# Kernel tuning notes

Hardware: AMD Instinct MI355X
Metric: run time of the kernel (lower is better)

## Reference

```python
import jax, jax.numpy as jnp
import numpy as np

NUM_HEADS = 16
HEAD_DIM = 64  # hidden_size 1024 / 16 heads


def setup_inputs() -> dict:
    key = jax.random.key(0)
    ks = jax.random.split(key, 4)
    B, S, H = 2, 2048, 1024
    scale = 0.02
    return {
        "hidden_states": jax.random.normal(ks[0], (B, S, H), jnp.float32),
        "attention_mask": jnp.zeros((B, 1, 1, S), jnp.float32),  # additive mask
        "Wq": jax.random.normal(ks[1], (H, H), jnp.float32) * scale,
        "bq": jnp.zeros((H,), jnp.float32),
        "Wk": jax.random.normal(ks[2], (H, H), jnp.float32) * scale,
        "bk": jnp.zeros((H,), jnp.float32),
        "Wv": jax.random.normal(ks[3], (H, H), jnp.float32) * scale,
        "bv": jnp.zeros((H,), jnp.float32),
    }


def _split_heads(x):
    B, S, H = x.shape
    return x.reshape(B, S, NUM_HEADS, HEAD_DIM).transpose(0, 2, 1, 3)  # [B,h,S,dh]


def reference(hidden_states, attention_mask, Wq, bq, Wk, bk, Wv, bv):
    q = _split_heads(hidden_states @ Wq + bq)
    k = _split_heads(hidden_states @ Wk + bk)
    v = _split_heads(hidden_states @ Wv + bv)
    # scaled dot-product scores [B,h,S,S]
    scores = jnp.einsum("bhqd,bhkd->bhqk", q, k) / np.sqrt(HEAD_DIM).astype(np.float32)
    scores = scores + attention_mask  # additive mask, broadcast [B,1,1,S]
    probs = jax.nn.softmax(scores, axis=-1)  # dropout prob = 0.0
    ctx = jnp.einsum("bhqk,bhkd->bhqd", probs, v)
    B, h, S, dh = ctx.shape
    return ctx.transpose(0, 2, 1, 3).reshape(B, S, h * dh)  # [B,S,hidden]
```

## Files before the change

### kernel.cpp

```cpp
#include <hip/hip_runtime.h>
#include <hip/hip_bf16.h>


typedef __bf16 bf16x8 __attribute__((ext_vector_type(8)));
typedef __bf16 bf16x4 __attribute__((ext_vector_type(4)));
typedef float f32x4 __attribute__((ext_vector_type(4)));

static constexpr int H = 1024;
static constexpr int S = 2048;
static constexpr int NH = 16;
static constexpr int DH = 64;
static constexpr float L2E = 1.4426950408889634f;

#if __has_builtin(__builtin_amdgcn_exp2f)
#define EXP2F(x) __builtin_amdgcn_exp2f(x)
#else
#define EXP2F(x) __builtin_exp2f(x)
#endif

__device__ inline void gll16(const void* g, void* l) {
  __builtin_amdgcn_global_load_lds(
      (const __attribute__((address_space(1))) void*)g,
      (__attribute__((address_space(3))) void*)l, 16, 0, 0);
}

__global__ __launch_bounds__(256) void convert_kernel(
    const float* __restrict__ X, const float* __restrict__ W0,
    const float* __restrict__ W1, const float* __restrict__ W2,
    __bf16* __restrict__ Xb, __bf16* __restrict__ Wt) {
  __shared__ float T[64][65];
  const int bid = blockIdx.x, tid = threadIdx.x;
  if (bid < 2048) {
    size_t i = ((size_t)bid * 256 + tid) * 8;
    float4 f0 = *(const float4*)(X + i);
    float4 f1 = *(const float4*)(X + i + 4);
    bf16x8 o;
    o[0] = (__bf16)f0.x; o[1] = (__bf16)f0.y; o[2] = (__bf16)f0.z; o[3] = (__bf16)f0.w;
    o[4] = (__bf16)f1.x; o[5] = (__bf16)f1.y; o[6] = (__bf16)f1.z; o[7] = (__bf16)f1.w;
    *(bf16x8*)(Xb + i) = o;
    return;
  }
  const int wid = bid - 2048;
  const int z = wid >> 8, t = wid & 255;
  const int k0 = (t >> 4) * 64, n0 = (t & 15) * 64;
  const float* W = z == 0 ? W0 : (z == 1 ? W1 : W2);
  __bf16* Wo = Wt + (size_t)z * H * H;
#pragma unroll
  for (int it = 0; it < 4; ++it) {
    int r = it * 16 + (tid >> 4), c = (tid & 15) * 4;
    *(float4*)&T[r][c] = *(const float4*)&W[(size_t)(k0 + r) * H + n0 + c];
  }
  __syncthreads();
#pragma unroll
  for (int it = 0; it < 4; ++it) {
    int n = it * 16 + (tid >> 4), c0 = (tid & 15) * 4;
    bf16x4 o;
#pragma unroll
    for (int j = 0; j < 4; ++j) o[j] = (__bf16)T[c0 + j][n];
    *(bf16x4*)&Wo[(size_t)(n0 + n) * H + k0 + c0] = o;
  }
}

__global__ __launch_bounds__(256, 3) void qkv_gemm_kernel(
    const __bf16* __restrict__ Xb, const __bf16* __restrict__ Wt,
    const float* __restrict__ bq, const float* __restrict__ bk,
    const float* __restrict__ bv,
    __bf16* __restrict__ Q, __bf16* __restrict__ K, __bf16* __restrict__ Vt)
{
  __shared__ __bf16 smem[2 * 128 * 64];
  __bf16* As = smem;
  __bf16* Bs = smem + 128 * 64;

  const int tid = threadIdx.x, lane = tid & 63, w = tid >> 6;
  const int quad = lane >> 4, l16 = lane & 15;
  const int wsel = blockIdx.x >> 3;
  const int n0 = (blockIdx.x & 7) * 128;
  const int m0 = blockIdx.y * 128;
  const int wr = w & 1, wc = w >> 1;

  const __bf16* Wsel = Wt + (size_t)wsel * H * H;
  const float* bias = wsel == 0 ? bq : (wsel == 1 ? bk : bv);

  const __bf16* aptr[4];
  const __bf16* bptr[4];
#pragma unroll
  for (int i = 0; i < 4; ++i) {
    int s = w * 256 + i * 64 + lane;
    int row = s >> 3, col = s & 7, sc = col ^ (row & 7);
    aptr[i] = Xb + (size_t)(m0 + row) * H + sc * 8;
    bptr[i] = Wsel + (size_t)(n0 + row) * H + sc * 8;
  }

  f32x4 acc[4][4];
#pragma unroll
  for (int u = 0; u < 4; ++u) {
    float bv_ = bias[n0 + wc * 64 + u * 16 + l16];
#pragma unroll
    for (int t = 0; t < 4; ++t) acc[t][u] = {bv_, bv_, bv_, bv_};
  }

  for (int k0 = 0; k0 < H; k0 += 64) {
    __syncthreads();
#pragma unroll
    for (int i = 0; i < 4; ++i) {
      gll16(aptr[i] + k0, &As[(w * 256 + i * 64) * 8]);
      gll16(bptr[i] + k0, &Bs[(w * 256 + i * 64) * 8]);
    }
    __syncthreads();
#pragma unroll
    for (int kc = 0; kc < 2; ++kc) {
      bf16x8 af[4], bfr[4];
#pragma unroll
      for (int t = 0; t < 4; ++t) {
        int ra = wr * 64 + t * 16 + l16;
        af[t] = *(const bf16x8*)&As[ra * 64 + (((kc * 4 + quad) ^ (ra & 7)) * 8)];
        int rb = wc * 64 + t * 16 + l16;
        bfr[t] = *(const bf16x8*)&Bs[rb * 64 + (((kc * 4 + quad) ^ (rb & 7)) * 8)];
      }
#pragma unroll
      for (int t = 0; t < 4; ++t)
#pragma unroll
        for (int u = 0; u < 4; ++u)
          acc[t][u] = __builtin_amdgcn_mfma_f32_16x16x32_bf16(af[t], bfr[u], acc[t][u], 0, 0, 0);
    }
  }

  const int b = m0 >> 11;
  if (wsel <= 1) {
    __syncthreads();
    __bf16* Tr = smem + w * (64 * 64);
    const float scl = wsel == 0 ? 0.125f * L2E : 1.0f;
#pragma unroll
    for (int t = 0; t < 4; ++t)
#pragma unroll
      for (int u = 0; u < 4; ++u)
#pragma unroll
        for (int r = 0; r < 4; ++r) {
          int row = t * 16 + quad * 4 + r;
          int col = u * 16 + l16;
          Tr[row * 64 + (((col >> 3) ^ (row & 7)) * 8 + (col & 7))] =
              (__bf16)(acc[t][u][r] * scl);
        }
    const int head = (n0 + wc * 64) >> 6;
    const int bh = b * NH + head;
    const int si = (m0 & (S - 1)) + wr * 64 + lane;
    __bf16* dst = (wsel == 0 ? Q : K) + ((size_t)bh * S + si) * DH;
#pragma unroll
    for (int c = 0; c < 8; ++c)
      *(bf16x8*)&dst[c * 8] =
          *(const bf16x8*)&Tr[lane * 64 + ((c ^ (lane & 7)) * 8)];
  } else {
#pragma unroll
    for (int u = 0; u < 4; ++u) {
      int n = n0 + wc * 64 + u * 16 + l16;
      int head = n >> 6, d = n & 63;
#pragma unroll
      for (int t = 0; t < 4; ++t) {
        int srow = m0 + wr * 64 + t * 16 + quad * 4;
        int si = srow & (S - 1);
        int bh = b * NH + head;
        bf16x4 o;
#pragma unroll
        for (int r = 0; r < 4; ++r) o[r] = (__bf16)acc[t][u][r];
        *(bf16x4*)&Vt[((size_t)bh * DH + d) * S + si] = o;
      }
    }
  }
}

__global__ __launch_bounds__(512, 4) void attn_kernel(
    const __bf16* __restrict__ Q, const __bf16* __restrict__ K,
    const __bf16* __restrict__ Vt, const float* __restrict__ mask,
    float* __restrict__ out)
{
  __shared__ __bf16 Ks[128 * 64];
  __shared__ __bf16 Vs[64 * 128];
  __shared__ float  Ms[S];
  __shared__ __bf16 Pb[8][16][128];

  const int tid = threadIdx.x, lane = tid & 63, w = tid >> 6;
  const int quad = lane >> 4, l16 = lane & 15;
  const int bh = blockIdx.y, b = bh >> 4, h = bh & 15;
  const int q0 = blockIdx.x * 128;

  const __bf16* Qb = Q + (size_t)bh * S * DH;
  const __bf16* Kb = K + (size_t)bh * S * DH;
  const __bf16* Vb = Vt + (size_t)bh * DH * S;
  const float* mb = mask + (size_t)b * S;

  {
    int idx = tid * 4;
    float4 mv = *(const float4*)&mb[idx];
    float4 sv = {mv.x * L2E, mv.y * L2E, mv.z * L2E, mv.w * L2E};
    *(float4*)&Ms[idx] = sv;
  }

  const int q = q0 + w * 16 + l16;
  bf16x8 qf[2];
#pragma unroll
  for (int kc = 0; kc < 2; ++kc)
    qf[kc] = *(const bf16x8*)&Qb[(size_t)q * DH + kc * 32 + quad * 8];

  bf16x8 ones_frag;
#pragma unroll
  for (int j = 0; j < 8; ++j) ones_frag[j] = (l16 == 0) ? (__bf16)1.0f : (__bf16)0.0f;

  const __bf16* kptr[2];
  const __bf16* vptr[2];
#pragma unroll
  for (int i = 0; i < 2; ++i) {
    int s = i * 512 + tid;
    {
      int row = s >> 3, col = s & 7, sc = col ^ (row & 7);
      kptr[i] = Kb + (size_t)row * DH + sc * 8;
    }
    {
      int row = s >> 4, col = s & 15, sc = col ^ (row & 15);
      vptr[i] = Vb + (size_t)row * S + sc * 8;
    }
  }

  f32x4 o[4] = {};
  f32x4 o4 = {};

  for (int kv0 = 0; kv0 < S; kv0 += 128) {
    __syncthreads();
#pragma unroll
    for (int i = 0; i < 2; ++i) {
      gll16(kptr[i] + (size_t)kv0 * DH, &Ks[(i * 512 + w * 64) * 8]);
      gll16(vptr[i] + kv0, &Vs[(i * 512 + w * 64) * 8]);
    }
    __syncthreads();

#pragma unroll
    for (int t = 0; t < 8; ++t) {
      int rk = t * 16 + l16;
      bf16x8 k0f = *(const bf16x8*)&Ks[rk * 64 + ((quad ^ (rk & 7)) * 8)];
      bf16x8 k1f = *(const bf16x8*)&Ks[rk * 64 + (((4 + quad) ^ (rk & 7)) * 8)];
      float4 m4 = *(const float4*)&Ms[kv0 + t * 16 + quad * 4];
      f32x4 z = {m4.x, m4.y, m4.z, m4.w};
      z = __builtin_amdgcn_mfma_f32_16x16x32_bf16(k0f, qf[0], z, 0, 0, 0);
      f32x4 sc = __builtin_amdgcn_mfma_f32_16x16x32_bf16(k1f, qf[1], z, 0, 0, 0);
      bf16x4 pk;
#pragma unroll
      for (int r = 0; r < 4; ++r) pk[r] = (__bf16)EXP2F(sc[r]);
      int col = t * 16 + quad * 4;
      *(bf16x4*)&Pb[w][l16][(((col >> 3) ^ l16) & 15) * 8 + (col & 7)] = pk;
    }

#pragma unroll
    for (int tt = 0; tt < 4; ++tt) {
      bf16x8 pf = *(const bf16x8*)&Pb[w][l16][(((tt * 4 + quad) ^ l16) & 15) * 8];
#pragma unroll
      for (int u = 0; u < 4; ++u) {
        int d = u * 16 + l16;
        bf16x8 vf = *(const bf16x8*)&Vs[d * 128 + (((4 * tt + quad) ^ l16) * 8)];
        o[u] = __builtin_amdgcn_mfma_f32_16x16x32_bf16(vf, pf, o[u], 0, 0, 0);
      }
      o4 = __builtin_amdgcn_mfma_f32_16x16x32_bf16(ones_frag, pf, o4, 0, 0, 0);
    }
  }

  float l_q = __shfl(o4[0], l16, 64);
  float invl = 1.0f / l_q;
#pragma unroll
  for (int u = 0; u < 4; ++u) {
    float4 st = {o[u][0] * invl, o[u][1] * invl, o[u][2] * invl, o[u][3] * invl};
    *(float4*)&out[((size_t)b * S + q) * H + h * DH + u * 16 + quad * 4] = st;
  }
}

extern "C" void kernel_launch(void* const* d_in, const int* in_sizes, int n_in,
                              void* d_out, int out_size, void* d_ws, size_t ws_size,
                              hipStream_t stream) {
  const float* X    = (const float*)d_in[0];
  const float* mask = (const float*)d_in[1];
  const float* Wq   = (const float*)d_in[2];
  const float* bq   = (const float*)d_in[3];
  const float* Wk   = (const float*)d_in[4];
  const float* bk   = (const float*)d_in[5];
  const float* Wv   = (const float*)d_in[6];
  const float* bv   = (const float*)d_in[7];
  float* out = (float*)d_out;

  const size_t per = (size_t)2 * NH * S * DH;
  __bf16* Qws  = (__bf16*)d_ws;
  __bf16* Kws  = Qws + per;
  __bf16* Vtws = Kws + per;

  __bf16* Xb = (__bf16*)d_out;
  __bf16* Wt = Xb + per;

  convert_kernel<<<2816, 256, 0, stream>>>(X, Wq, Wk, Wv, Xb, Wt);
  qkv_gemm_kernel<<<dim3(24, 32), 256, 0, stream>>>(Xb, Wt, bq, bk, bv,
                                                    Qws, Kws, Vtws);
  attn_kernel<<<dim3(16, 32), 512, 0, stream>>>(Qws, Kws, Vtws, mask, out);
}
```

Baseline: 170.3 us.

## Process two query tiles per wave to reuse K/V fragments in attention

The attention kernel drops from 8 waves of 16 queries to 4 waves of 32 queries each, so every K and V fragment read from LDS feeds two MFMAs instead of one. The mask is now read straight from global memory each tile instead of being staged in LDS. The goal is to halve LDS fragment traffic per MFMA and reduce block size. The cost is more registers per thread, fewer waves per block for hiding latency, and redundant global mask loads.

```diff
diff --git a/kernel.cpp b/kernel.cpp
--- a/kernel.cpp
+++ b/kernel.cpp
@@ -168,15 +168,14 @@
   }
 }
 
-__global__ __launch_bounds__(512, 4) void attn_kernel(
+__global__ __launch_bounds__(256, 2) void attn_kernel(
     const __bf16* __restrict__ Q, const __bf16* __restrict__ K,
     const __bf16* __restrict__ Vt, const float* __restrict__ mask,
     float* __restrict__ out)
 {
   __shared__ __bf16 Ks[128 * 64];
   __shared__ __bf16 Vs[64 * 128];
-  __shared__ float  Ms[S];
-  __shared__ __bf16 Pb[8][16][128];
+  __shared__ __bf16 Pb[4 * 32 * 128];
 
   const int tid = threadIdx.x, lane = tid & 63, w = tid >> 6;
   const int quad = lane >> 4, l16 = lane & 15;
@@ -188,85 +187,94 @@
   const __bf16* Vb = Vt + (size_t)bh * DH * S;
   const float* mb = mask + (size_t)b * S;
 
-  {
-    int idx = tid * 4;
-    float4 mv = *(const float4*)&mb[idx];
-    float4 sv = {mv.x * L2E, mv.y * L2E, mv.z * L2E, mv.w * L2E};
-    *(float4*)&Ms[idx] = sv;
-  }
-
-  const int q = q0 + w * 16 + l16;
-  bf16x8 qf[2];
-#pragma unroll
-  for (int kc = 0; kc < 2; ++kc)
-    qf[kc] = *(const bf16x8*)&Qb[(size_t)q * DH + kc * 32 + quad * 8];
+  bf16x8 qf[2][2];
+#pragma unroll
+  for (int qh = 0; qh < 2; ++qh) {
+    int q = q0 + w * 32 + qh * 16 + l16;
+#pragma unroll
+    for (int kc = 0; kc < 2; ++kc)
+      qf[qh][kc] = *(const bf16x8*)&Qb[(size_t)q * DH + kc * 32 + quad * 8];
+  }
 
   bf16x8 ones_frag;
 #pragma unroll
   for (int j = 0; j < 8; ++j) ones_frag[j] = (l16 == 0) ? (__bf16)1.0f : (__bf16)0.0f;
 
-  const __bf16* kptr[2];
-  const __bf16* vptr[2];
-#pragma unroll
-  for (int i = 0; i < 2; ++i) {
-    int s = i * 512 + tid;
-    {
-      int row = s >> 3, col = s & 7, sc = col ^ (row & 7);
-      kptr[i] = Kb + (size_t)row * DH + sc * 8;
-    }
-    {
-      int row = s >> 4, col = s & 15, sc = col ^ (row & 15);
-      vptr[i] = Vb + (size_t)row * S + sc * 8;
-    }
-  }
-
-  f32x4 o[4] = {};
-  f32x4 o4 = {};
+  const __bf16* kp[4];
+  const __bf16* vp[4];
+#pragma unroll
+  for (int i = 0; i < 4; ++i) {
+    int s = i * 256 + tid;
+    int rk = s >> 3, ck = s & 7;
+    kp[i] = Kb + (size_t)rk * DH + ((ck ^ (rk & 7)) * 8);
+    int rv = s >> 4, cv = s & 15;
+    vp[i] = Vb + (size_t)rv * S + ((cv ^ (rv & 15)) * 8);
+  }
+
+  f32x4 o[2][4] = {};
+  f32x4 o4[2] = {};
 
   for (int kv0 = 0; kv0 < S; kv0 += 128) {
     __syncthreads();
 #pragma unroll
-    for (int i = 0; i < 2; ++i) {
-      gll16(kptr[i] + (size_t)kv0 * DH, &Ks[(i * 512 + w * 64) * 8]);
-      gll16(vptr[i] + kv0, &Vs[(i * 512 + w * 64) * 8]);
+    for (int i = 0; i < 4; ++i) {
+      gll16(kp[i] + (size_t)kv0 * DH, &Ks[(i * 256 + w * 64) * 8]);
+      gll16(vp[i] + kv0, &Vs[(i * 256 + w * 64) * 8]);
     }
     __syncthreads();
 
 #pragma unroll
     for (int t = 0; t < 8; ++t) {
       int rk = t * 16 + l16;
-      bf16x8 k0f = *(const bf16x8*)&Ks[rk * 64 + ((quad ^ (rk & 7)) * 8)];
-      bf16x8 k1f = *(const bf16x8*)&Ks[rk * 64 + (((4 + quad) ^ (rk & 7)) * 8)];
-      float4 m4 = *(const float4*)&Ms[kv0 + t * 16 + quad * 4];
-      f32x4 z = {m4.x, m4.y, m4.z, m4.w};
-      z = __builtin_amdgcn_mfma_f32_16x16x32_bf16(k0f, qf[0], z, 0, 0, 0);
-      f32x4 sc = __builtin_amdgcn_mfma_f32_16x16x32_bf16(k1f, qf[1], z, 0, 0, 0);
-      bf16x4 pk;
-#pragma unroll
-      for (int r = 0; r < 4; ++r) pk[r] = (__bf16)EXP2F(sc[r]);
-      int col = t * 16 + quad * 4;
-      *(bf16x4*)&Pb[w][l16][(((col >> 3) ^ l16) & 15) * 8 + (col & 7)] = pk;
-    }
-
-#pragma unroll
-    for (int tt = 0; tt < 4; ++tt) {
-      bf16x8 pf = *(const bf16x8*)&Pb[w][l16][(((tt * 4 + quad) ^ l16) & 15) * 8];
+      bf16x8 k0f = *(const bf16x8*)&Ks[(rk * 8 + (quad ^ (rk & 7))) * 8];
+      bf16x8 k1f = *(const bf16x8*)&Ks[(rk * 8 + ((4 + quad) ^ (rk & 7))) * 8];
+      float4 mv = *(const float4*)&mb[kv0 + t * 16 + quad * 4];
+      int c3 = 2 * t + (quad >> 1);
+#pragma unroll
+      for (int qh = 0; qh < 2; ++qh) {
+        f32x4 z = {mv.x * L2E, mv.y * L2E, mv.z * L2E, mv.w * L2E};
+        z = __builtin_amdgcn_mfma_f32_16x16x32_bf16(k0f, qf[qh][0], z, 0, 0, 0);
+        f32x4 sc = __builtin_amdgcn_mfma_f32_16x16x32_bf16(k1f, qf[qh][1], z, 0, 0, 0);
+        bf16x4 pk;
+#pragma unroll
+        for (int r = 0; r < 4; ++r) pk[r] = (__bf16)EXP2F(sc[r]);
+        *(bf16x4*)&Pb[(w * 32 + qh * 16 + l16) * 128 +
+                      ((c3 ^ l16) & 15) * 8 + (quad & 1) * 4] = pk;
+      }
+    }
+
+#pragma unroll
+    for (int kc = 0; kc < 4; ++kc) {
+      bf16x8 pf[2];
+#pragma unroll
+      for (int qh = 0; qh < 2; ++qh)
+        pf[qh] = *(const bf16x8*)&Pb[(w * 32 + qh * 16 + l16) * 128 +
+                                     (((4 * kc + quad) ^ l16) & 15) * 8];
 #pragma unroll
       for (int u = 0; u < 4; ++u) {
         int d = u * 16 + l16;
-        bf16x8 vf = *(const bf16x8*)&Vs[d * 128 + (((4 * tt + quad) ^ l16) * 8)];
-        o[u] = __builtin_amdgcn_mfma_f32_16x16x32_bf16(vf, pf, o[u], 0, 0, 0);
+        bf16x8 vf = *(const bf16x8*)&Vs[(d * 16 + (((4 * kc + quad) ^ l16) & 15)) * 8];
+#pragma unroll
+        for (int qh = 0; qh < 2; ++qh)
+          o[qh][u] = __builtin_amdgcn_mfma_f32_16x16x32_bf16(vf, pf[qh], o[qh][u], 0, 0, 0);
       }
-      o4 = __builtin_amdgcn_mfma_f32_16x16x32_bf16(ones_frag, pf, o4, 0, 0, 0);
-    }
-  }
-
-  float l_q = __shfl(o4[0], l16, 64);
-  float invl = 1.0f / l_q;
-#pragma unroll
-  for (int u = 0; u < 4; ++u) {
-    float4 st = {o[u][0] * invl, o[u][1] * invl, o[u][2] * invl, o[u][3] * invl};
-    *(float4*)&out[((size_t)b * S + q) * H + h * DH + u * 16 + quad * 4] = st;
+#pragma unroll
+      for (int qh = 0; qh < 2; ++qh)
+        o4[qh] = __builtin_amdgcn_mfma_f32_16x16x32_bf16(ones_frag, pf[qh], o4[qh], 0, 0, 0);
+    }
+  }
+
+#pragma unroll
+  for (int qh = 0; qh < 2; ++qh) {
+    float l_q = __shfl(o4[qh][0], l16, 64);
+    float invl = 1.0f / l_q;
+    int q = q0 + w * 32 + qh * 16 + l16;
+#pragma unroll
+    for (int u = 0; u < 4; ++u) {
+      float4 st = {o[qh][u][0] * invl, o[qh][u][1] * invl,
+                   o[qh][u][2] * invl, o[qh][u][3] * invl};
+      *(float4*)&out[((size_t)b * S + q) * H + h * DH + u * 16 + quad * 4] = st;
+    }
   }
 }
 
@@ -294,5 +302,5 @@
   convert_kernel<<<2816, 256, 0, stream>>>(X, Wq, Wk, Wv, Xb, Wt);
   qkv_gemm_kernel<<<dim3(24, 32), 256, 0, stream>>>(Xb, Wt, bq, bk, bv,
                                                     Qws, Kws, Vtws);
-  attn_kernel<<<dim3(16, 32), 512, 0, stream>>>(Qws, Kws, Vtws, mask, out);
-}
+  attn_kernel<<<dim3(16, 32), 256, 0, stream>>>(Qws, Kws, Vtws, mask, out);
+}
```

New measurement: 180.5 us. 1.06x slower.

## Split KV tile across two wave groups with 32-query waves and merge partials

Applied to the files above, without the earlier changes.

Each wave now handles 32 queries and half of each 128-key tile. K fragments are reused across two query sub-tiles and V fragments across both query halves, which halves LDS fragment reads per MFMA. The two wave groups' partial outputs and row sums are combined through shared memory at the end. The row sum is now accumulated in fp32 registers with cross-lane shuffles instead of a ones-MFMA. The mask is read directly from global memory instead of being staged in LDS. This costs extra registers, a final LDS reduction, and more global mask loads.

```diff
diff --git a/kernel.cpp b/kernel.cpp
--- a/kernel.cpp
+++ b/kernel.cpp
@@ -173,13 +173,14 @@
     const __bf16* __restrict__ Vt, const float* __restrict__ mask,
     float* __restrict__ out)
 {
-  __shared__ __bf16 Ks[128 * 64];
-  __shared__ __bf16 Vs[64 * 128];
-  __shared__ float  Ms[S];
-  __shared__ __bf16 Pb[8][16][128];
+  __shared__ __align__(16) char pool[65536];
+  __bf16* Ks = (__bf16*)pool;
+  __bf16* Vs = (__bf16*)(pool + 16384);
+  __bf16* Pb = (__bf16*)(pool + 32768);
 
   const int tid = threadIdx.x, lane = tid & 63, w = tid >> 6;
   const int quad = lane >> 4, l16 = lane & 15;
+  const int gq = w & 3, g = w >> 2;
   const int bh = blockIdx.y, b = bh >> 4, h = bh & 15;
   const int q0 = blockIdx.x * 128;
 
@@ -188,22 +189,14 @@
   const __bf16* Vb = Vt + (size_t)bh * DH * S;
   const float* mb = mask + (size_t)b * S;
 
-  {
-    int idx = tid * 4;
-    float4 mv = *(const float4*)&mb[idx];
-    float4 sv = {mv.x * L2E, mv.y * L2E, mv.z * L2E, mv.w * L2E};
-    *(float4*)&Ms[idx] = sv;
-  }
-
-  const int q = q0 + w * 16 + l16;
-  bf16x8 qf[2];
-#pragma unroll
-  for (int kc = 0; kc < 2; ++kc)
-    qf[kc] = *(const bf16x8*)&Qb[(size_t)q * DH + kc * 32 + quad * 8];
-
-  bf16x8 ones_frag;
-#pragma unroll
-  for (int j = 0; j < 8; ++j) ones_frag[j] = (l16 == 0) ? (__bf16)1.0f : (__bf16)0.0f;
+  bf16x8 qf[2][2];
+#pragma unroll
+  for (int qh = 0; qh < 2; ++qh) {
+    int q = q0 + gq * 32 + qh * 16 + l16;
+#pragma unroll
+    for (int kc = 0; kc < 2; ++kc)
+      qf[qh][kc] = *(const bf16x8*)&Qb[(size_t)q * DH + kc * 32 + quad * 8];
+  }
 
   const __bf16* kptr[2];
   const __bf16* vptr[2];
@@ -220,8 +213,10 @@
     }
   }
 
-  f32x4 o[4] = {};
-  f32x4 o4 = {};
+  __bf16* Pw = Pb + (size_t)w * 32 * 64;
+
+  f32x4 o[2][4] = {};
+  float l_acc[2] = {0.f, 0.f};
 
   for (int kv0 = 0; kv0 < S; kv0 += 128) {
     __syncthreads();
@@ -232,41 +227,96 @@
     }
     __syncthreads();
 
-#pragma unroll
-    for (int t = 0; t < 8; ++t) {
-      int rk = t * 16 + l16;
+    const int kvh = kv0 + g * 64;
+
+#pragma unroll
+    for (int mt = 0; mt < 4; ++mt) {
+      int rk = g * 64 + mt * 16 + l16;
       bf16x8 k0f = *(const bf16x8*)&Ks[rk * 64 + ((quad ^ (rk & 7)) * 8)];
       bf16x8 k1f = *(const bf16x8*)&Ks[rk * 64 + (((4 + quad) ^ (rk & 7)) * 8)];
-      float4 m4 = *(const float4*)&Ms[kv0 + t * 16 + quad * 4];
-      f32x4 z = {m4.x, m4.y, m4.z, m4.w};
-      z = __builtin_amdgcn_mfma_f32_16x16x32_bf16(k0f, qf[0], z, 0, 0, 0);
-      f32x4 sc = __builtin_amdgcn_mfma_f32_16x16x32_bf16(k1f, qf[1], z, 0, 0, 0);
-      bf16x4 pk;
-#pragma unroll
-      for (int r = 0; r < 4; ++r) pk[r] = (__bf16)EXP2F(sc[r]);
-      int col = t * 16 + quad * 4;
-      *(bf16x4*)&Pb[w][l16][(((col >> 3) ^ l16) & 15) * 8 + (col & 7)] = pk;
-    }
-
-#pragma unroll
-    for (int tt = 0; tt < 4; ++tt) {
-      bf16x8 pf = *(const bf16x8*)&Pb[w][l16][(((tt * 4 + quad) ^ l16) & 15) * 8];
-#pragma unroll
-      for (int u = 0; u < 4; ++u) {
-        int d = u * 16 + l16;
-        bf16x8 vf = *(const bf16x8*)&Vs[d * 128 + (((4 * tt + quad) ^ l16) * 8)];
-        o[u] = __builtin_amdgcn_mfma_f32_16x16x32_bf16(vf, pf, o[u], 0, 0, 0);
-      }
-      o4 = __builtin_amdgcn_mfma_f32_16x16x32_bf16(ones_frag, pf, o4, 0, 0, 0);
-    }
-  }
-
-  float l_q = __shfl(o4[0], l16, 64);
-  float invl = 1.0f / l_q;
-#pragma unroll
-  for (int u = 0; u < 4; ++u) {
-    float4 st = {o[u][0] * invl, o[u][1] * invl, o[u][2] * invl, o[u][3] * invl};
-    *(float4*)&out[((size_t)b * S + q) * H + h * DH + u * 16 + quad * 4] = st;
+      float4 mv = *(const float4*)&mb[kvh + mt * 16 + quad * 4];
+      f32x4 z0 = {mv.x * L2E, mv.y * L2E, mv.z * L2E, mv.w * L2E};
+#pragma unroll
+      for (int qh = 0; qh < 2; ++qh) {
+        f32x4 z = __builtin_amdgcn_mfma_f32_16x16x32_bf16(k0f, qf[qh][0], z0, 0, 0, 0);
+        f32x4 sc = __builtin_amdgcn_mfma_f32_16x16x32_bf16(k1f, qf[qh][1], z, 0, 0, 0);
+        bf16x4 pk;
+#pragma unroll
+        for (int r = 0; r < 4; ++r) {
+          float p = EXP2F(sc[r]);
+          l_acc[qh] += p;
+          pk[r] = (__bf16)p;
+        }
+        int q = qh * 16 + l16;
+        int key = (q & 7) ^ ((q >> 3) & 3);
+        int ch = mt * 2 + (quad >> 1);
+        *(bf16x4*)&Pw[q * 64 + ((ch ^ key) * 8 + (quad & 1) * 4)] = pk;
+      }
+    }
+
+#pragma unroll
+    for (int kc = 0; kc < 2; ++kc) {
+      bf16x8 pf[2];
+#pragma unroll
+      for (int qh = 0; qh < 2; ++qh) {
+        int q = qh * 16 + l16;
+        int key = (q & 7) ^ ((q >> 3) & 3);
+        pf[qh] = *(const bf16x8*)&Pw[q * 64 + (((kc * 4 + quad) ^ key) * 8)];
+      }
+#pragma unroll
+      for (int mt = 0; mt < 4; ++mt) {
+        int d = mt * 16 + l16;
+        int ch = g * 8 + kc * 4 + quad;
+        bf16x8 vf = *(const bf16x8*)&Vs[d * 128 + ((ch ^ (d & 15)) * 8)];
+#pragma unroll
+        for (int qh = 0; qh < 2; ++qh)
+          o[qh][mt] = __builtin_amdgcn_mfma_f32_16x16x32_bf16(vf, pf[qh], o[qh][mt], 0, 0, 0);
+      }
+    }
+  }
+
+  float l_half[2];
+#pragma unroll
+  for (int qh = 0; qh < 2; ++qh) {
+    float l = l_acc[qh];
+    l += __shfl_xor(l, 16, 64);
+    l += __shfl_xor(l, 32, 64);
+    l_half[qh] = l;
+  }
+
+  __syncthreads();
+  if (g == 1) {
+    float4* mo = (float4*)pool;
+    int base = ((w - 4) * 64 + lane) * 8;
+#pragma unroll
+    for (int qh = 0; qh < 2; ++qh)
+#pragma unroll
+      for (int mt = 0; mt < 4; ++mt) {
+        float4 v = {o[qh][mt][0], o[qh][mt][1], o[qh][mt][2], o[qh][mt][3]};
+        mo[base + qh * 4 + mt] = v;
+      }
+    float* ml = (float*)(pool + 32768);
+    ml[((w - 4) * 64 + lane) * 2 + 0] = l_half[0];
+    ml[((w - 4) * 64 + lane) * 2 + 1] = l_half[1];
+  }
+  __syncthreads();
+  if (g == 0) {
+    float4* mo = (float4*)pool;
+    float* ml = (float*)(pool + 32768);
+    int base = (w * 64 + lane) * 8;
+#pragma unroll
+    for (int qh = 0; qh < 2; ++qh) {
+      float l_q = l_half[qh] + ml[(w * 64 + lane) * 2 + qh];
+      float invl = 1.0f / l_q;
+      int q = q0 + gq * 32 + qh * 16 + l16;
+#pragma unroll
+      for (int mt = 0; mt < 4; ++mt) {
+        float4 p = mo[base + qh * 4 + mt];
+        float4 st = {(o[qh][mt][0] + p.x) * invl, (o[qh][mt][1] + p.y) * invl,
+                     (o[qh][mt][2] + p.z) * invl, (o[qh][mt][3] + p.w) * invl};
+        *(float4*)&out[((size_t)b * S + q) * H + h * DH + mt * 16 + quad * 4] = st;
+      }
+    }
   }
 }
 
```

New measurement: 183.0 us. +7.4%, slower.
